# Performance work log

Hardware: AMD Instinct MI355X
Metric: run time of the kernel (lower is better)

Reference implementation:

```python
import jax, jax.numpy as jnp
import numpy as np

NDIGIT = 10
DIM_IN = 256
DIM_OUT = 784
BATCH = 16384


def setup_inputs() -> dict:
    key = jax.random.key(0)
    k_theta, k_label, k_W = jax.random.split(key, 3)
    theta = jax.random.normal(k_theta, (BATCH, DIM_IN), dtype=jnp.float32)
    label = jax.random.randint(k_label, (BATCH,), 0, NDIGIT, dtype=jnp.int32)
    # xavier_uniform for each (dim_out, dim_in) matrix
    limit = float(np.sqrt(6.0 / (DIM_IN + DIM_OUT)))
    megaW = jax.random.uniform(k_W, (NDIGIT, DIM_OUT, DIM_IN), dtype=jnp.float32,
                               minval=-limit, maxval=limit)
    megab = jnp.zeros((NDIGIT, DIM_OUT), dtype=jnp.float32)
    return {"theta": theta, "label": label, "megaW": megaW, "megab": megab}


def reference(theta, label, megaW, megab):
    # Dense compute across all 10 digit experts (matches torch.bmm over repeated theta)
    # added: [b, ndigit, dim_out]
    added = jnp.einsum('ndi,bi->bnd', megaW, theta) + megab[None, :, :]
    # Select the expert output per example by label (vector_gather)
    selected = jnp.take_along_axis(added, label[:, None, None].astype(jnp.int32), axis=1)[:, 0, :]
    probs = jax.nn.sigmoid(selected)
    return probs
```

## Files before the change

### kernel.cpp

```cpp
#include <hip/hip_runtime.h>
#include <hip/hip_bf16.h>

#define NDIGIT 10
#define DIM_IN 256
#define DIM_OUT 784
#define BATCH 16384
#define BM 64
#define BN 112
#define NCB 7
#define MAX_MT (BATCH / BM + NDIGIT)
#define GEMM_BLOCKS (MAX_MT * NCB)

#define WS_IDX 1024
#define WS_WBF_BYTES 69632

typedef __attribute__((ext_vector_type(4))) float f32x4;
typedef __attribute__((ext_vector_type(8))) short bf16x8;

__device__ __forceinline__ short f2bf(float f) {
    union { float f; unsigned u; } c; c.f = f;
    unsigned u = c.u;
    u += 0x7fffu + ((u >> 16) & 1u);
    return (short)(u >> 16);
}

__device__ __forceinline__ void gload16(const void* gp, void* lp) {
    __builtin_amdgcn_global_load_lds(
        (const __attribute__((address_space(1))) void*)gp,
        (__attribute__((address_space(3))) void*)lp, 16, 0, 0);
}

__global__ void prep_k(const float* __restrict__ megaW,
                       const int* __restrict__ label,
                       int* __restrict__ wsi,
                       short* __restrict__ wbf) {
    int b = blockIdx.x, t = threadIdx.x;
    if (b < 980) {
        int base = b * 2048 + t * 8;
        f32x4 v0 = *(const f32x4*)(megaW + base);
        f32x4 v1 = *(const f32x4*)(megaW + base + 4);
        bf16x8 o;
        o[0] = f2bf(v0[0]); o[1] = f2bf(v0[1]); o[2] = f2bf(v0[2]); o[3] = f2bf(v0[3]);
        o[4] = f2bf(v1[0]); o[5] = f2bf(v1[1]); o[6] = f2bf(v1[2]); o[7] = f2bf(v1[3]);
        *(bf16x8*)(wbf + base) = o;
    } else {
        __shared__ int h[NDIGIT];
        int j = b - 980;
        if (t < NDIGIT) h[t] = 0;
        __syncthreads();
        int i0 = j * 512;
        atomicAdd(&h[label[i0 + t]], 1);
        atomicAdd(&h[label[i0 + 256 + t]], 1);
        __syncthreads();
        if (t < NDIGIT) wsi[64 + j * 16 + t] = h[t];
    }
}

__global__ void scatter2_k(const int* __restrict__ label, int* __restrict__ wsi) {
    __shared__ int tot[NDIGIT], bef[NDIGIT], base[NDIGIT + 1], cur[NDIGIT];
    int j = blockIdx.x, t = threadIdx.x;
    if (t < NDIGIT) {
        int s = 0, sb = 0;
        for (int jj = 0; jj < 32; ++jj) {
            int v = wsi[64 + jj * 16 + t];
            s += v;
            if (jj < j) sb += v;
        }
        tot[t] = s; bef[t] = sb;
    }
    __syncthreads();
    if (t == 0) {
        int off = 0;
        for (int g = 0; g < NDIGIT; ++g) { base[g] = off; off += tot[g]; }
        base[NDIGIT] = off;
    }
    __syncthreads();
    if (t < NDIGIT) cur[t] = base[t] + bef[t];
    __syncthreads();
    int i = j * 512 + t;
    int g = label[i];
    int r = atomicAdd(&cur[g], 1);
    wsi[WS_IDX + r] = i;
    if (j == 0 && t == 0) {
        int off = 0, toff = 0;
        for (int g2 = 0; g2 < NDIGIT; ++g2) {
            wsi[g2] = off; wsi[12 + g2] = toff;
            off += tot[g2]; toff += (tot[g2] + BM - 1) / BM;
        }
        wsi[10] = off; wsi[22] = toff; wsi[24] = toff;
    }
}

__launch_bounds__(256, 4)
__global__ void moe_gemm4_k(const float* __restrict__ theta,
                            const float* __restrict__ megab,
                            const int* __restrict__ wsi,
                            const short* __restrict__ wbf,
                            float* __restrict__ out) {
    __shared__ short Bs[BN * 128];

    int Bid = blockIdx.x;
    const int q = GEMM_BLOCKS / 8, r = GEMM_BLOCKS % 8;
    int xcd = Bid & 7, slot = Bid >> 3;
    int w = (xcd < r ? xcd * (q + 1) : r * (q + 1) + (xcd - r) * q) + slot;
    int mt = w / NCB, cb = w % NCB;

    int total = wsi[24];
    if (mt >= total) return;

    int g = 0;
    while (mt >= wsi[12 + g + 1]) ++g;
    int lt    = mt - wsi[12 + g];
    int start = wsi[g];
    int cnt   = wsi[g + 1] - start;
    int row0  = lt * BM;
    int rc    = min(BM, cnt - row0);

    int tid = threadIdx.x;
    int wv = tid >> 6, l = tid & 63, r16 = l & 15, kg = l >> 4;

    const char* Wcb = (const char*)(wbf + ((size_t)g * DIM_OUT + (size_t)cb * BN) * DIM_IN);

#pragma unroll
    for (int it = 0; it < 7; ++it) {
        int lbyte = (it * 256 + tid) << 4;
        int L = lbyte ^ (((lbyte >> 8) & 7) << 4);
        int srcoff = ((L >> 8) << 9) + (L & 255);
        gload16(Wcb + srcoff, (char*)Bs + lbyte);
    }

    const int* idxlist = wsi + WS_IDX + start + row0;
    int mloc = wv * 16 + r16;
    int asrc = (mloc < rc) ? idxlist[mloc] : idxlist[0];
    const float* Arow = theta + (size_t)asrc * DIM_IN;
    bf16x8 a[8];
#pragma unroll
    for (int ks = 0; ks < 8; ++ks) {
        int k0 = ks * 32 + kg * 8;
        f32x4 v0 = *(const f32x4*)(Arow + k0);
        f32x4 v1 = *(const f32x4*)(Arow + k0 + 4);
        bf16x8 af;
        af[0] = f2bf(v0[0]); af[1] = f2bf(v0[1]);
        af[2] = f2bf(v0[2]); af[3] = f2bf(v0[3]);
        af[4] = f2bf(v1[0]); af[5] = f2bf(v1[1]);
        af[6] = f2bf(v1[2]); af[7] = f2bf(v1[3]);
        a[ks] = af;
    }

    f32x4 acc[NCB];
#pragma unroll
    for (int ns = 0; ns < NCB; ++ns) acc[ns] = (f32x4){0.f, 0.f, 0.f, 0.f};

    __syncthreads();
#pragma unroll
    for (int ks = 0; ks < 4; ++ks)
#pragma unroll
        for (int ns = 0; ns < NCB; ++ns) {
            int n = ns * 16 + r16;
            int byte = (n << 8) + (ks << 6) + (kg << 4);
            byte ^= (n & 7) << 4;
            bf16x8 b = *(const bf16x8*)((const char*)Bs + byte);
            acc[ns] = __builtin_amdgcn_mfma_f32_16x16x32_bf16(a[ks], b, acc[ns], 0, 0, 0);
        }
    __syncthreads();

#pragma unroll
    for (int it = 0; it < 7; ++it) {
        int lbyte = (it * 256 + tid) << 4;
        int L = lbyte ^ (((lbyte >> 8) & 7) << 4);
        int srcoff = ((L >> 8) << 9) + (L & 255) + 256;
        gload16(Wcb + srcoff, (char*)Bs + lbyte);
    }
    __syncthreads();

#pragma unroll
    for (int ks = 0; ks < 4; ++ks)
#pragma unroll
        for (int ns = 0; ns < NCB; ++ns) {
            int n = ns * 16 + r16;
            int byte = (n << 8) + (ks << 6) + (kg << 4);
            byte ^= (n & 7) << 4;
            bf16x8 b = *(const bf16x8*)((const char*)Bs + byte);
            acc[ns] = __builtin_amdgcn_mfma_f32_16x16x32_bf16(a[4 + ks], b, acc[ns], 0, 0, 0);
        }

    const float* bg = megab + (size_t)g * DIM_OUT + (size_t)cb * BN;
    int rbase = wv * 16 + kg * 4;
    int orow[4];
#pragma unroll
    for (int j = 0; j < 4; ++j)
        orow[j] = (rbase + j < rc) ? idxlist[rbase + j] : -1;

#pragma unroll
    for (int ns = 0; ns < NCB; ++ns) {
        int nloc = ns * 16 + r16;
        float bias = bg[nloc];
#pragma unroll
        for (int j = 0; j < 4; ++j) {
            if (orow[j] >= 0) {
                float x = acc[ns][j] + bias;
                out[(size_t)orow[j] * DIM_OUT + cb * BN + nloc] = 1.0f / (1.0f + __expf(-x));
            }
        }
    }
}

extern "C" void kernel_launch(void* const* d_in, const int* in_sizes, int n_in,
                              void* d_out, int out_size, void* d_ws, size_t ws_size,
                              hipStream_t stream) {
    const float* theta = (const float*)d_in[0];
    const int*   label = (const int*)d_in[1];
    const float* megaW = (const float*)d_in[2];
    const float* megab = (const float*)d_in[3];
    float* out = (float*)d_out;
    int* wsi = (int*)d_ws;
    short* wbf = (short*)((char*)d_ws + WS_WBF_BYTES);

    prep_k    <<<1012, 256, 0, stream>>>(megaW, label, wsi, wbf);
    scatter2_k<<<32, 512, 0, stream>>>(label, wsi);
    moe_gemm4_k<<<GEMM_BLOCKS, 256, 0, stream>>>(theta, megab, wsi, wbf, out);
}
```

Measured before the change: 47.83 us.

## Pre-gather theta to sorted bf16 and double-buffer W tiles in GEMM

Adds a kernel that gathers theta rows into label-sorted order and converts them to bf16 in workspace, so the GEMM reads contiguous bf16 A rows instead of converting fp32 in every N-column block. The GEMM splits K into four quarters staged through two LDS buffers, with explicit waitcnt and barriers so global-to-LDS loads overlap MFMA work. This costs an extra launch and an extra write and read of the sorted activations. The new path only runs when the workspace is large enough; otherwise it falls back to the old kernel.

```diff
diff --git a/kernel.cpp b/kernel.cpp
--- a/kernel.cpp
+++ b/kernel.cpp
@@ -10,9 +10,13 @@
 #define NCB 7
 #define MAX_MT (BATCH / BM + NDIGIT)
 #define GEMM_BLOCKS (MAX_MT * NCB)
+#define QBYTES 14336
 
 #define WS_IDX 1024
 #define WS_WBF_BYTES 69632
+#define WS_TH_BYTES (WS_WBF_BYTES + 2007040 * 2)
+#define WS_NEED_OLD (WS_TH_BYTES)
+#define WS_NEED_NEW (WS_TH_BYTES + BATCH * DIM_IN * 2)
 
 typedef __attribute__((ext_vector_type(4))) float f32x4;
 typedef __attribute__((ext_vector_type(8))) short bf16x8;
@@ -91,18 +95,61 @@
     }
 }
 
+__global__ void gth_k(const float* __restrict__ theta,
+                      const int* __restrict__ wsi,
+                      short* __restrict__ thsort) {
+    int gid = blockIdx.x * 256 + threadIdx.x;
+    int r = gid >> 5;
+    int c8 = (gid & 31) << 3;
+    int src = wsi[WS_IDX + r];
+    const float* p = theta + (size_t)src * DIM_IN + c8;
+    f32x4 v0 = *(const f32x4*)p;
+    f32x4 v1 = *(const f32x4*)(p + 4);
+    bf16x8 o;
+    o[0] = f2bf(v0[0]); o[1] = f2bf(v0[1]); o[2] = f2bf(v0[2]); o[3] = f2bf(v0[3]);
+    o[4] = f2bf(v1[0]); o[5] = f2bf(v1[1]); o[6] = f2bf(v1[2]); o[7] = f2bf(v1[3]);
+    *(bf16x8*)(thsort + (size_t)r * DIM_IN + c8) = o;
+}
+
+__device__ __forceinline__ void stage_q(const char* Wcb, int q, char* Bq, int tid) {
+#pragma unroll
+    for (int it = 0; it < 4; ++it) {
+        int chunk = it * 256 + tid;
+        if (chunk >= 896) chunk -= 128;
+        int lbyte = chunk << 4;
+        int L = lbyte ^ ((((lbyte >> 7) & 7)) << 4);
+        int row = L >> 7, koff = L & 127;
+        gload16(Wcb + row * 512 + q * 128 + koff, Bq + lbyte);
+    }
+}
+
+#define COMPUTE(Q, BUF) do { \
+    _Pragma("unroll") \
+    for (int ksl = 0; ksl < 2; ++ksl) { \
+        _Pragma("unroll") \
+        for (int ns = 0; ns < NCB; ++ns) { \
+            int n = ns * 16 + r16; \
+            int byte = (n << 7) + (ksl << 6) + (kg << 4); \
+            byte ^= (n & 7) << 4; \
+            bf16x8 bfr = *(const bf16x8*)((const char*)(BUF) + byte); \
+            acc[ns] = __builtin_amdgcn_mfma_f32_16x16x32_bf16(a[(Q) * 2 + ksl], bfr, acc[ns], 0, 0, 0); \
+        } \
+    } \
+} while (0)
+
 __launch_bounds__(256, 4)
-__global__ void moe_gemm4_k(const float* __restrict__ theta,
+__global__ void moe_gemm5_k(const short* __restrict__ thsort,
                             const float* __restrict__ megab,
                             const int* __restrict__ wsi,
                             const short* __restrict__ wbf,
                             float* __restrict__ out) {
-    __shared__ short Bs[BN * 128];
+    __shared__ char Bs0[QBYTES];
+    __shared__ char Bs1[QBYTES];
 
     int Bid = blockIdx.x;
-    const int q = GEMM_BLOCKS / 8, r = GEMM_BLOCKS % 8;
+    const int q8 = GEMM_BLOCKS / 8, r8 = GEMM_BLOCKS % 8;
     int xcd = Bid & 7, slot = Bid >> 3;
-    int w = (xcd < r ? xcd * (q + 1) : r * (q + 1) + (xcd - r) * q) + slot;
+    int w = (xcd < r8 ? xcd * (q8 + 1) : r8 * (q8 + 1) + (xcd - r8) * q8) + slot;
     int mt = w / NCB, cb = w % NCB;
 
     int total = wsi[24];
@@ -119,20 +166,108 @@
     int tid = threadIdx.x;
     int wv = tid >> 6, l = tid & 63, r16 = l & 15, kg = l >> 4;
 
+    int arow = start + row0 + wv * 16 + r16;
+    if (arow > BATCH - 1) arow = BATCH - 1;
+    const short* Ar = thsort + (size_t)arow * DIM_IN + kg * 8;
+    bf16x8 a[8];
+#pragma unroll
+    for (int ks = 0; ks < 8; ++ks)
+        a[ks] = *(const bf16x8*)(Ar + ks * 32);
+
+    const int* idxlist = wsi + WS_IDX + start + row0;
+    int rbase = wv * 16 + kg * 4;
+    int orow[4];
+#pragma unroll
+    for (int j = 0; j < 4; ++j)
+        orow[j] = (rbase + j < rc) ? idxlist[rbase + j] : -1;
+
     const char* Wcb = (const char*)(wbf + ((size_t)g * DIM_OUT + (size_t)cb * BN) * DIM_IN);
 
+    stage_q(Wcb, 0, Bs0, tid);
+    stage_q(Wcb, 1, Bs1, tid);
+
+    f32x4 acc[NCB];
+#pragma unroll
+    for (int ns = 0; ns < NCB; ++ns) acc[ns] = (f32x4){0.f, 0.f, 0.f, 0.f};
+
+    asm volatile("s_waitcnt vmcnt(4)" ::: "memory");
+    __builtin_amdgcn_s_barrier();
+    __builtin_amdgcn_sched_barrier(0);
+
+    COMPUTE(0, Bs0);
+    asm volatile("s_waitcnt lgkmcnt(0)" ::: "memory");
+    __builtin_amdgcn_s_barrier();
+    stage_q(Wcb, 2, Bs0, tid);
+    asm volatile("s_waitcnt vmcnt(4)" ::: "memory");
+    __builtin_amdgcn_s_barrier();
+    __builtin_amdgcn_sched_barrier(0);
+
+    COMPUTE(1, Bs1);
+    asm volatile("s_waitcnt lgkmcnt(0)" ::: "memory");
+    __builtin_amdgcn_s_barrier();
+    stage_q(Wcb, 3, Bs1, tid);
+    asm volatile("s_waitcnt vmcnt(4)" ::: "memory");
+    __builtin_amdgcn_s_barrier();
+    __builtin_amdgcn_sched_barrier(0);
+
+    COMPUTE(2, Bs0);
+    asm volatile("s_waitcnt lgkmcnt(0) vmcnt(0)" ::: "memory");
+    __builtin_amdgcn_s_barrier();
+    __builtin_amdgcn_sched_barrier(0);
+
+    COMPUTE(3, Bs1);
+
+    const float* bg = megab + (size_t)g * DIM_OUT + (size_t)cb * BN;
+#pragma unroll
+    for (int ns = 0; ns < NCB; ++ns) {
+        int nloc = ns * 16 + r16;
+        float bias = bg[nloc];
+#pragma unroll
+        for (int j = 0; j < 4; ++j) {
+            if (orow[j] >= 0) {
+                float x = acc[ns][j] + bias;
+                out[(size_t)orow[j] * DIM_OUT + cb * BN + nloc] = 1.0f / (1.0f + __expf(-x));
+            }
+        }
+    }
+}
+
+__launch_bounds__(256, 4)
+__global__ void moe_gemm4_k(const float* __restrict__ theta,
+                            const float* __restrict__ megab,
+                            const int* __restrict__ wsi,
+                            const short* __restrict__ wbf,
+                            float* __restrict__ out) {
+    __shared__ short Bsf[BN * 128];
+    int Bid = blockIdx.x;
+    const int q8 = GEMM_BLOCKS / 8, r8 = GEMM_BLOCKS % 8;
+    int xcd = Bid & 7, slot = Bid >> 3;
+    int w = (xcd < r8 ? xcd * (q8 + 1) : r8 * (q8 + 1) + (xcd - r8) * q8) + slot;
+    int mt = w / NCB, cb = w % NCB;
+    int total = wsi[24];
+    if (mt >= total) return;
+    int g = 0;
+    while (mt >= wsi[12 + g + 1]) ++g;
+    int lt    = mt - wsi[12 + g];
+    int start = wsi[g];
+    int cnt   = wsi[g + 1] - start;
+    int row0  = lt * BM;
+    int rc    = min(BM, cnt - row0);
+    int tid = threadIdx.x;
+    int wv = tid >> 6, l = tid & 63, r16 = l & 15, kg = l >> 4;
+    const char* Wcb = (const char*)(wbf + ((size_t)g * DIM_OUT + (size_t)cb * BN) * DIM_IN);
 #pragma unroll
     for (int it = 0; it < 7; ++it) {
         int lbyte = (it * 256 + tid) << 4;
         int L = lbyte ^ (((lbyte >> 8) & 7) << 4);
         int srcoff = ((L >> 8) << 9) + (L & 255);
-        gload16(Wcb + srcoff, (char*)Bs + lbyte);
-    }
-
+        gload16(Wcb + srcoff, (char*)Bsf + lbyte);
+    }
     const int* idxlist = wsi + WS_IDX + start + row0;
     int mloc = wv * 16 + r16;
     int asrc = (mloc < rc) ? idxlist[mloc] : idxlist[0];
-    const float* Arow = theta + (size_t)asrc * DIM_IN;
+    const float* Arow = (const float*)0;
+    Arow = theta + (size_t)asrc * DIM_IN;
     bf16x8 a[8];
 #pragma unroll
     for (int ks = 0; ks < 8; ++ks) {
@@ -146,11 +281,9 @@
         af[6] = f2bf(v1[2]); af[7] = f2bf(v1[3]);
         a[ks] = af;
     }
-
     f32x4 acc[NCB];
 #pragma unroll
     for (int ns = 0; ns < NCB; ++ns) acc[ns] = (f32x4){0.f, 0.f, 0.f, 0.f};
-
     __syncthreads();
 #pragma unroll
     for (int ks = 0; ks < 4; ++ks)
@@ -159,20 +292,18 @@
             int n = ns * 16 + r16;
             int byte = (n << 8) + (ks << 6) + (kg << 4);
             byte ^= (n & 7) << 4;
-            bf16x8 b = *(const bf16x8*)((const char*)Bs + byte);
+            bf16x8 b = *(const bf16x8*)((const char*)Bsf + byte);
             acc[ns] = __builtin_amdgcn_mfma_f32_16x16x32_bf16(a[ks], b, acc[ns], 0, 0, 0);
         }
     __syncthreads();
-
 #pragma unroll
     for (int it = 0; it < 7; ++it) {
         int lbyte = (it * 256 + tid) << 4;
         int L = lbyte ^ (((lbyte >> 8) & 7) << 4);
         int srcoff = ((L >> 8) << 9) + (L & 255) + 256;
-        gload16(Wcb + srcoff, (char*)Bs + lbyte);
-    }
-    __syncthreads();
-
+        gload16(Wcb + srcoff, (char*)Bsf + lbyte);
+    }
+    __syncthreads();
 #pragma unroll
     for (int ks = 0; ks < 4; ++ks)
 #pragma unroll
@@ -180,17 +311,15 @@
             int n = ns * 16 + r16;
             int byte = (n << 8) + (ks << 6) + (kg << 4);
             byte ^= (n & 7) << 4;
-            bf16x8 b = *(const bf16x8*)((const char*)Bs + byte);
+            bf16x8 b = *(const bf16x8*)((const char*)Bsf + byte);
             acc[ns] = __builtin_amdgcn_mfma_f32_16x16x32_bf16(a[4 + ks], b, acc[ns], 0, 0, 0);
         }
-
     const float* bg = megab + (size_t)g * DIM_OUT + (size_t)cb * BN;
     int rbase = wv * 16 + kg * 4;
     int orow[4];
 #pragma unroll
     for (int j = 0; j < 4; ++j)
         orow[j] = (rbase + j < rc) ? idxlist[rbase + j] : -1;
-
 #pragma unroll
     for (int ns = 0; ns < NCB; ++ns) {
         int nloc = ns * 16 + r16;
@@ -218,5 +347,12 @@
 
     prep_k    <<<1012, 256, 0, stream>>>(megaW, label, wsi, wbf);
     scatter2_k<<<32, 512, 0, stream>>>(label, wsi);
-    moe_gemm4_k<<<GEMM_BLOCKS, 256, 0, stream>>>(theta, megab, wsi, wbf, out);
-}
+
+    if (ws_size >= (size_t)WS_NEED_NEW) {
+        short* thsort = (short*)((char*)d_ws + WS_TH_BYTES);
+        gth_k     <<<2048, 256, 0, stream>>>(theta, wsi, thsort);
+        moe_gemm5_k<<<GEMM_BLOCKS, 256, 0, stream>>>(thsort, megab, wsi, wbf, out);
+    } else {
+        moe_gemm4_k<<<GEMM_BLOCKS, 256, 0, stream>>>(theta, megab, wsi, wbf, out);
+    }
+}
```

After: 47.19 us. Within noise of the previous version (-1.3%).

## Pre-gather theta to sorted bf16 and reuse full-K weight tile across 256 rows

Applied to the files above, without the earlier changes.

Adds a gather kernel that writes theta rows in label-sorted order as bf16, then a new GEMM kernel where each block keeps both K-halves of a 112-column weight slice in double LDS buffers. That slice is reused across four 64-row subtiles (256 rows), with register double-buffering of A loads and epilogue overlap. This cuts repeated weight staging and per-block fp32 theta conversion, but costs an extra kernel launch, an extra pass over theta, and lower occupancy. It falls back to the old kernel when the workspace is too small.

```diff
diff --git a/kernel.cpp b/kernel.cpp
--- a/kernel.cpp
+++ b/kernel.cpp
@@ -10,9 +10,14 @@
 #define NCB 7
 #define MAX_MT (BATCH / BM + NDIGIT)
 #define GEMM_BLOCKS (MAX_MT * NCB)
+#define MAX_CHUNKS (BATCH / 256 + NDIGIT)
+#define G6_BLOCKS (MAX_CHUNKS * NCB)
+#define HBYTES 28672
 
 #define WS_IDX 1024
 #define WS_WBF_BYTES 69632
+#define WS_TH_BYTES (WS_WBF_BYTES + 2007040 * 2)
+#define WS_NEED_NEW (WS_TH_BYTES + BATCH * DIM_IN * 2)
 
 typedef __attribute__((ext_vector_type(4))) float f32x4;
 typedef __attribute__((ext_vector_type(8))) short bf16x8;
@@ -82,13 +87,178 @@
     int r = atomicAdd(&cur[g], 1);
     wsi[WS_IDX + r] = i;
     if (j == 0 && t == 0) {
-        int off = 0, toff = 0;
+        int off = 0, toff = 0, choff = 0;
         for (int g2 = 0; g2 < NDIGIT; ++g2) {
-            wsi[g2] = off; wsi[12 + g2] = toff;
-            off += tot[g2]; toff += (tot[g2] + BM - 1) / BM;
+            wsi[g2] = off; wsi[12 + g2] = toff; wsi[26 + g2] = choff;
+            off += tot[g2];
+            toff += (tot[g2] + BM - 1) / BM;
+            choff += (tot[g2] + 255) / 256;
         }
         wsi[10] = off; wsi[22] = toff; wsi[24] = toff;
-    }
+        wsi[36] = choff; wsi[38] = choff;
+    }
+}
+
+__global__ void gth_k(const float* __restrict__ theta,
+                      const int* __restrict__ wsi,
+                      short* __restrict__ thsort) {
+    int gid = blockIdx.x * 256 + threadIdx.x;
+    int r = gid >> 5;
+    int c8 = (gid & 31) << 3;
+    int src = wsi[WS_IDX + r];
+    const float* p = theta + (size_t)src * DIM_IN + c8;
+    f32x4 v0 = *(const f32x4*)p;
+    f32x4 v1 = *(const f32x4*)(p + 4);
+    bf16x8 o;
+    o[0] = f2bf(v0[0]); o[1] = f2bf(v0[1]); o[2] = f2bf(v0[2]); o[3] = f2bf(v0[3]);
+    o[4] = f2bf(v1[0]); o[5] = f2bf(v1[1]); o[6] = f2bf(v1[2]); o[7] = f2bf(v1[3]);
+    *(bf16x8*)(thsort + (size_t)r * DIM_IN + c8) = o;
+}
+
+
+#define LOADA(A, T) do {                                                       \
+    int arow_ = start + row0 + (T) * 64 + wv * 16 + r16;                       \
+    int amax_ = start + cnt - 1;                                               \
+    if (arow_ > amax_) arow_ = amax_;                                          \
+    const short* Ar_ = thsort + (size_t)arow_ * DIM_IN + kg * 8;               \
+    _Pragma("unroll")                                                          \
+    for (int ks = 0; ks < 8; ++ks) (A)[ks] = *(const bf16x8*)(Ar_ + ks * 32);  \
+} while (0)
+
+#define LOADO(O, T) do {                                                       \
+    const int* idxl_ = wsi + WS_IDX + start + row0 + (T) * 64;                 \
+    _Pragma("unroll")                                                          \
+    for (int j = 0; j < 4; ++j) {                                              \
+        int rl_ = (T) * 64 + rb + j;                                           \
+        (O)[j] = (rl_ < cnt - row0) ? idxl_[rb + j] : -1;                      \
+    }                                                                          \
+} while (0)
+
+#define CMPH(H, A, BUF) do {                                                   \
+    _Pragma("unroll")                                                          \
+    for (int ksl = 0; ksl < 4; ++ksl) {                                        \
+        _Pragma("unroll")                                                      \
+        for (int ns = 0; ns < NCB; ++ns) {                                     \
+            int n_ = ns * 16 + r16;                                            \
+            int byte_ = (n_ << 8) + (ksl << 6) + (kg << 4);                    \
+            byte_ ^= (n_ & 7) << 4;                                            \
+            bf16x8 bfr_ = *(const bf16x8*)((const char*)(BUF) + byte_);        \
+            acc[ns] = __builtin_amdgcn_mfma_f32_16x16x32_bf16(                 \
+                (A)[(H) * 4 + ksl], bfr_, acc[ns], 0, 0, 0);                   \
+        }                                                                      \
+    }                                                                          \
+} while (0)
+
+#define ZACC() do {                                                            \
+    _Pragma("unroll")                                                          \
+    for (int ns = 0; ns < NCB; ++ns) acc[ns] = (f32x4){0.f, 0.f, 0.f, 0.f};   \
+} while (0)
+
+#define EPI(O) do {                                                            \
+    _Pragma("unroll")                                                          \
+    for (int ns = 0; ns < NCB; ++ns) {                                         \
+        int nloc_ = ns * 16 + r16;                                             \
+        _Pragma("unroll")                                                      \
+        for (int j = 0; j < 4; ++j) {                                          \
+            if ((O)[j] >= 0) {                                                 \
+                float x_ = acc[ns][j] + biasv[ns];                             \
+                out[(size_t)(O)[j] * DIM_OUT + cb * BN + nloc_] =              \
+                    1.0f / (1.0f + __expf(-x_));                               \
+            }                                                                  \
+        }                                                                      \
+    }                                                                          \
+} while (0)
+
+#define STAGEH(H, BUF) do {                                                    \
+    _Pragma("unroll")                                                          \
+    for (int it = 0; it < 7; ++it) {                                           \
+        int lbyte_ = (it * 256 + tid) << 4;                                    \
+        int L_ = lbyte_ ^ (((lbyte_ >> 8) & 7) << 4);                          \
+        int src_ = ((L_ >> 8) << 9) + (L_ & 255) + (H) * 256;                  \
+        gload16(Wcb + src_, (char*)(BUF) + lbyte_);                            \
+    }                                                                          \
+} while (0)
+
+__launch_bounds__(256, 2)
+__global__ void moe_gemm6_k(const short* __restrict__ thsort,
+                            const float* __restrict__ megab,
+                            const int* __restrict__ wsi,
+                            const short* __restrict__ wbf,
+                            float* __restrict__ out) {
+    __shared__ char Bs0[HBYTES];
+    __shared__ char Bs1[HBYTES];
+
+    int Bid = blockIdx.x;
+    const int q8 = G6_BLOCKS / 8, r8 = G6_BLOCKS % 8;
+    int xcd = Bid & 7, slot = Bid >> 3;
+    int w = (xcd < r8 ? xcd * (q8 + 1) : r8 * (q8 + 1) + (xcd - r8) * q8) + slot;
+    int ct = w / NCB, cb = w % NCB;
+
+    int ctotal = wsi[38];
+    if (ct >= ctotal) return;
+
+    int tid = threadIdx.x;
+    int wv = tid >> 6, l = tid & 63, r16 = l & 15, kg = l >> 4;
+    int rb = wv * 16 + kg * 4;
+
+    int coff = (l < 11) ? wsi[26 + l] : 0x7fffffff;
+    int boff = (l < 11) ? wsi[l] : 0;
+    unsigned long long m = __ballot(ct >= coff);
+    int g = __popcll(m) - 1;
+    int lc    = ct - __shfl(coff, g);
+    int start = __shfl(boff, g);
+    int cnt   = __shfl(boff, g + 1) - start;
+    int row0  = lc * 256;
+
+    const char* Wcb = (const char*)(wbf + ((size_t)g * DIM_OUT + (size_t)cb * BN) * DIM_IN);
+
+    bf16x8 a0[8], a1[8];
+    int or0[4], or1[4];
+    LOADA(a0, 0);
+    LOADO(or0, 0);
+    float biasv[NCB];
+    {
+        const float* bg = megab + (size_t)g * DIM_OUT + cb * BN;
+#pragma unroll
+        for (int ns = 0; ns < NCB; ++ns) biasv[ns] = bg[ns * 16 + r16];
+    }
+
+    STAGEH(0, Bs0);
+    STAGEH(1, Bs1);
+
+    f32x4 acc[NCB];
+    ZACC();
+
+    asm volatile("s_waitcnt vmcnt(7)" ::: "memory");
+    __builtin_amdgcn_s_barrier();
+    __builtin_amdgcn_sched_barrier(0);
+
+    CMPH(0, a0, Bs0);
+
+    asm volatile("s_waitcnt vmcnt(0)" ::: "memory");
+    __builtin_amdgcn_s_barrier();
+    __builtin_amdgcn_sched_barrier(0);
+
+    LOADA(a1, 1); LOADO(or1, 1);
+    CMPH(1, a0, Bs1);
+    EPI(or0);
+
+    ZACC();
+    LOADA(a0, 2); LOADO(or0, 2);
+    CMPH(0, a1, Bs0);
+    CMPH(1, a1, Bs1);
+    EPI(or1);
+
+    ZACC();
+    LOADA(a1, 3); LOADO(or1, 3);
+    CMPH(0, a0, Bs0);
+    CMPH(1, a0, Bs1);
+    EPI(or0);
+
+    ZACC();
+    CMPH(0, a1, Bs0);
+    CMPH(1, a1, Bs1);
+    EPI(or1);
 }
 
 __launch_bounds__(256, 4)
@@ -97,17 +267,14 @@
                             const int* __restrict__ wsi,
                             const short* __restrict__ wbf,
                             float* __restrict__ out) {
-    __shared__ short Bs[BN * 128];
-
+    __shared__ short Bsf[BN * 128];
     int Bid = blockIdx.x;
-    const int q = GEMM_BLOCKS / 8, r = GEMM_BLOCKS % 8;
+    const int q8 = GEMM_BLOCKS / 8, r8 = GEMM_BLOCKS % 8;
     int xcd = Bid & 7, slot = Bid >> 3;
-    int w = (xcd < r ? xcd * (q + 1) : r * (q + 1) + (xcd - r) * q) + slot;
+    int w = (xcd < r8 ? xcd * (q8 + 1) : r8 * (q8 + 1) + (xcd - r8) * q8) + slot;
     int mt = w / NCB, cb = w % NCB;
-
     int total = wsi[24];
     if (mt >= total) return;
-
     int g = 0;
     while (mt >= wsi[12 + g + 1]) ++g;
     int lt    = mt - wsi[12 + g];
@@ -115,20 +282,16 @@
     int cnt   = wsi[g + 1] - start;
     int row0  = lt * BM;
     int rc    = min(BM, cnt - row0);
-
     int tid = threadIdx.x;
     int wv = tid >> 6, l = tid & 63, r16 = l & 15, kg = l >> 4;
-
     const char* Wcb = (const char*)(wbf + ((size_t)g * DIM_OUT + (size_t)cb * BN) * DIM_IN);
-
 #pragma unroll
     for (int it = 0; it < 7; ++it) {
         int lbyte = (it * 256 + tid) << 4;
         int L = lbyte ^ (((lbyte >> 8) & 7) << 4);
         int srcoff = ((L >> 8) << 9) + (L & 255);
-        gload16(Wcb + srcoff, (char*)Bs + lbyte);
-    }
-
+        gload16(Wcb + srcoff, (char*)Bsf + lbyte);
+    }
     const int* idxlist = wsi + WS_IDX + start + row0;
     int mloc = wv * 16 + r16;
     int asrc = (mloc < rc) ? idxlist[mloc] : idxlist[0];
@@ -146,11 +309,9 @@
         af[6] = f2bf(v1[2]); af[7] = f2bf(v1[3]);
         a[ks] = af;
     }
-
     f32x4 acc[NCB];
 #pragma unroll
     for (int ns = 0; ns < NCB; ++ns) acc[ns] = (f32x4){0.f, 0.f, 0.f, 0.f};
-
     __syncthreads();
 #pragma unroll
     for (int ks = 0; ks < 4; ++ks)
@@ -159,20 +320,18 @@
             int n = ns * 16 + r16;
             int byte = (n << 8) + (ks << 6) + (kg << 4);
             byte ^= (n & 7) << 4;
-            bf16x8 b = *(const bf16x8*)((const char*)Bs + byte);
+            bf16x8 b = *(const bf16x8*)((const char*)Bsf + byte);
             acc[ns] = __builtin_amdgcn_mfma_f32_16x16x32_bf16(a[ks], b, acc[ns], 0, 0, 0);
         }
     __syncthreads();
-
 #pragma unroll
     for (int it = 0; it < 7; ++it) {
         int lbyte = (it * 256 + tid) << 4;
         int L = lbyte ^ (((lbyte >> 8) & 7) << 4);
         int srcoff = ((L >> 8) << 9) + (L & 255) + 256;
-        gload16(Wcb + srcoff, (char*)Bs + lbyte);
-    }
-    __syncthreads();
-
+        gload16(Wcb + srcoff, (char*)Bsf + lbyte);
+    }
+    __syncthreads();
 #pragma unroll
     for (int ks = 0; ks < 4; ++ks)
 #pragma unroll
@@ -180,17 +339,15 @@
             int n = ns * 16 + r16;
             int byte = (n << 8) + (ks << 6) + (kg << 4);
             byte ^= (n & 7) << 4;
-            bf16x8 b = *(const bf16x8*)((const char*)Bs + byte);
+            bf16x8 b = *(const bf16x8*)((const char*)Bsf + byte);
             acc[ns] = __builtin_amdgcn_mfma_f32_16x16x32_bf16(a[4 + ks], b, acc[ns], 0, 0, 0);
         }
-
     const float* bg = megab + (size_t)g * DIM_OUT + (size_t)cb * BN;
     int rbase = wv * 16 + kg * 4;
     int orow[4];
 #pragma unroll
     for (int j = 0; j < 4; ++j)
         orow[j] = (rbase + j < rc) ? idxlist[rbase + j] : -1;
-
 #pragma unroll
     for (int ns = 0; ns < NCB; ++ns) {
         int nloc = ns * 16 + r16;
@@ -218,5 +375,12 @@
 
     prep_k    <<<1012, 256, 0, stream>>>(megaW, label, wsi, wbf);
     scatter2_k<<<32, 512, 0, stream>>>(label, wsi);
-    moe_gemm4_k<<<GEMM_BLOCKS, 256, 0, stream>>>(theta, megab, wsi, wbf, out);
-}
+
+    if (ws_size >= (size_t)WS_NEED_NEW) {
+        short* thsort = (short*)((char*)d_ws + WS_TH_BYTES);
+        gth_k     <<<2048, 256, 0, stream>>>(theta, wsi, thsort);
+        moe_gemm6_k<<<G6_BLOCKS, 256, 0, stream>>>(thsort, megab, wsi, wbf, out);
+    } else {
+        moe_gemm4_k<<<GEMM_BLOCKS, 256, 0, stream>>>(theta, megab, wsi, wbf, out);
+    }
+}
```

Result: slower. 74.36 us (+55.5%).

## Pre-gather sorted bf16 theta, precompute tile descriptors, stage W in quarters

Applied to the files above, without the earlier changes.

Adds a gather kernel that writes theta rows in label-sorted order as bf16, so the GEMM reads contiguous half-size A rows instead of converting fp32 per tile, which each of the 7 column blocks repeated. scatter2 now writes a packed per-tile descriptor, so the GEMM no longer loops to find its expert. The W tile is staged in four 14KB K-quarters to cut LDS use, and launch bounds are raised to 8 blocks per CU for occupancy. The cost is an extra kernel launch, a round trip through workspace memory, and more barriers per tile.

```diff
diff --git a/kernel.cpp b/kernel.cpp
--- a/kernel.cpp
+++ b/kernel.cpp
@@ -9,10 +9,13 @@
 #define BN 112
 #define NCB 7
 #define MAX_MT (BATCH / BM + NDIGIT)
-#define GEMM_BLOCKS (MAX_MT * NCB)
+#define G9_BLOCKS (MAX_MT * NCB)
+#define QB 14336
 
 #define WS_IDX 1024
+#define WS_DESC 600
 #define WS_WBF_BYTES 69632
+#define WS_TH_BYTES (WS_WBF_BYTES + 2007040 * 2)
 
 typedef __attribute__((ext_vector_type(4))) float f32x4;
 typedef __attribute__((ext_vector_type(8))) short bf16x8;
@@ -57,7 +60,7 @@
 }
 
 __global__ void scatter2_k(const int* __restrict__ label, int* __restrict__ wsi) {
-    __shared__ int tot[NDIGIT], bef[NDIGIT], base[NDIGIT + 1], cur[NDIGIT];
+    __shared__ int tot[NDIGIT], bef[NDIGIT], base[NDIGIT + 1], cur[NDIGIT], toff[NDIGIT + 1];
     int j = blockIdx.x, t = threadIdx.x;
     if (t < NDIGIT) {
         int s = 0, sb = 0;
@@ -70,126 +73,131 @@
     }
     __syncthreads();
     if (t == 0) {
-        int off = 0;
-        for (int g = 0; g < NDIGIT; ++g) { base[g] = off; off += tot[g]; }
-        base[NDIGIT] = off;
+        int off = 0, tf = 0;
+        for (int g = 0; g < NDIGIT; ++g) {
+            base[g] = off; toff[g] = tf;
+            off += tot[g]; tf += (tot[g] + BM - 1) / BM;
+        }
+        base[NDIGIT] = off; toff[NDIGIT] = tf;
     }
     __syncthreads();
     if (t < NDIGIT) cur[t] = base[t] + bef[t];
+    if (j == 0) {
+        int ptotal = toff[NDIGIT];
+        for (int p = t; p < ptotal; p += 512) {
+            int g2 = 0;
+            while (p >= toff[g2 + 1]) ++g2;
+            int row0 = (p - toff[g2]) * BM;
+            int rcv = tot[g2] - row0; if (rcv > BM) rcv = BM;
+            wsi[WS_DESC + p] = (base[g2] + row0) | (rcv << 14) | (g2 << 21);
+        }
+        if (t == 0) wsi[24] = ptotal;
+    }
     __syncthreads();
     int i = j * 512 + t;
     int g = label[i];
     int r = atomicAdd(&cur[g], 1);
     wsi[WS_IDX + r] = i;
-    if (j == 0 && t == 0) {
-        int off = 0, toff = 0;
-        for (int g2 = 0; g2 < NDIGIT; ++g2) {
-            wsi[g2] = off; wsi[12 + g2] = toff;
-            off += tot[g2]; toff += (tot[g2] + BM - 1) / BM;
-        }
-        wsi[10] = off; wsi[22] = toff; wsi[24] = toff;
-    }
-}
-
-__launch_bounds__(256, 4)
-__global__ void moe_gemm4_k(const float* __restrict__ theta,
+    if (j == 0 && t < NDIGIT) wsi[t] = base[t];
+    if (j == 0 && t == 0) wsi[10] = base[NDIGIT];
+}
+
+__global__ void gth_k(const float* __restrict__ theta,
+                      const int* __restrict__ wsi,
+                      short* __restrict__ thsort) {
+    int gid = blockIdx.x * 256 + threadIdx.x;
+    int r = gid >> 5;
+    int c8 = (gid & 31) << 3;
+    int src = wsi[WS_IDX + r];
+    const float* p = theta + (size_t)src * DIM_IN + c8;
+    f32x4 v0 = *(const f32x4*)p;
+    f32x4 v1 = *(const f32x4*)(p + 4);
+    bf16x8 o;
+    o[0] = f2bf(v0[0]); o[1] = f2bf(v0[1]); o[2] = f2bf(v0[2]); o[3] = f2bf(v0[3]);
+    o[4] = f2bf(v1[0]); o[5] = f2bf(v1[1]); o[6] = f2bf(v1[2]); o[7] = f2bf(v1[3]);
+    *(bf16x8*)(thsort + (size_t)r * DIM_IN + c8) = o;
+}
+
+__device__ __forceinline__ void stage_q(const char* Wcb, int q, char* Bq, int tid) {
+#pragma unroll
+    for (int it = 0; it < 4; ++it) {
+        int chunk = it * 256 + tid;
+        if (chunk >= 896) chunk -= 128;
+        int lbyte = chunk << 4;
+        int L = lbyte ^ ((((lbyte >> 7) & 7)) << 4);
+        int row = L >> 7, koff = L & 127;
+        gload16(Wcb + row * 512 + q * 128 + koff, Bq + lbyte);
+    }
+}
+
+#define COMPUTE(Q) do {                                                        \
+    _Pragma("unroll")                                                          \
+    for (int ksl = 0; ksl < 2; ++ksl) {                                        \
+        _Pragma("unroll")                                                      \
+        for (int ns = 0; ns < NCB; ++ns) {                                     \
+            int n_ = ns * 16 + r16;                                            \
+            int byte_ = (n_ << 7) + (ksl << 6) + (kg << 4);                    \
+            byte_ ^= (n_ & 7) << 4;                                            \
+            bf16x8 bfr_ = *(const bf16x8*)(Bs + byte_);                        \
+            acc[ns] = __builtin_amdgcn_mfma_f32_16x16x32_bf16(                 \
+                a[(Q) * 2 + ksl], bfr_, acc[ns], 0, 0, 0);                     \
+        }                                                                      \
+    }                                                                          \
+} while (0)
+
+__launch_bounds__(256, 8)
+__global__ void moe_gemm9_k(const short* __restrict__ thsort,
                             const float* __restrict__ megab,
                             const int* __restrict__ wsi,
                             const short* __restrict__ wbf,
                             float* __restrict__ out) {
-    __shared__ short Bs[BN * 128];
+    __shared__ char Bs[QB];
 
     int Bid = blockIdx.x;
-    const int q = GEMM_BLOCKS / 8, r = GEMM_BLOCKS % 8;
+    const int q8 = G9_BLOCKS / 8, r8 = G9_BLOCKS % 8;
     int xcd = Bid & 7, slot = Bid >> 3;
-    int w = (xcd < r ? xcd * (q + 1) : r * (q + 1) + (xcd - r) * q) + slot;
+    int w = (xcd < r8 ? xcd * (q8 + 1) : r8 * (q8 + 1) + (xcd - r8) * q8) + slot;
     int mt = w / NCB, cb = w % NCB;
 
     int total = wsi[24];
     if (mt >= total) return;
 
-    int g = 0;
-    while (mt >= wsi[12 + g + 1]) ++g;
-    int lt    = mt - wsi[12 + g];
-    int start = wsi[g];
-    int cnt   = wsi[g + 1] - start;
-    int row0  = lt * BM;
-    int rc    = min(BM, cnt - row0);
+    int d = wsi[WS_DESC + mt];
+    int startRow = d & 0x3FFF;
+    int rc = (d >> 14) & 0x7F;
+    int g  = d >> 21;
 
     int tid = threadIdx.x;
     int wv = tid >> 6, l = tid & 63, r16 = l & 15, kg = l >> 4;
 
+    int mloc = wv * 16 + r16; if (mloc >= rc) mloc = rc - 1;
+    const short* Ar = thsort + (size_t)(startRow + mloc) * DIM_IN + kg * 8;
+    bf16x8 a[8];
+#pragma unroll
+    for (int ks = 0; ks < 8; ++ks)
+        a[ks] = *(const bf16x8*)(Ar + ks * 32);
+
     const char* Wcb = (const char*)(wbf + ((size_t)g * DIM_OUT + (size_t)cb * BN) * DIM_IN);
 
-#pragma unroll
-    for (int it = 0; it < 7; ++it) {
-        int lbyte = (it * 256 + tid) << 4;
-        int L = lbyte ^ (((lbyte >> 8) & 7) << 4);
-        int srcoff = ((L >> 8) << 9) + (L & 255);
-        gload16(Wcb + srcoff, (char*)Bs + lbyte);
-    }
-
-    const int* idxlist = wsi + WS_IDX + start + row0;
-    int mloc = wv * 16 + r16;
-    int asrc = (mloc < rc) ? idxlist[mloc] : idxlist[0];
-    const float* Arow = theta + (size_t)asrc * DIM_IN;
-    bf16x8 a[8];
-#pragma unroll
-    for (int ks = 0; ks < 8; ++ks) {
-        int k0 = ks * 32 + kg * 8;
-        f32x4 v0 = *(const f32x4*)(Arow + k0);
-        f32x4 v1 = *(const f32x4*)(Arow + k0 + 4);
-        bf16x8 af;
-        af[0] = f2bf(v0[0]); af[1] = f2bf(v0[1]);
-        af[2] = f2bf(v0[2]); af[3] = f2bf(v0[3]);
-        af[4] = f2bf(v1[0]); af[5] = f2bf(v1[1]);
-        af[6] = f2bf(v1[2]); af[7] = f2bf(v1[3]);
-        a[ks] = af;
-    }
-
     f32x4 acc[NCB];
 #pragma unroll
     for (int ns = 0; ns < NCB; ++ns) acc[ns] = (f32x4){0.f, 0.f, 0.f, 0.f};
 
-    __syncthreads();
-#pragma unroll
-    for (int ks = 0; ks < 4; ++ks)
-#pragma unroll
-        for (int ns = 0; ns < NCB; ++ns) {
-            int n = ns * 16 + r16;
-            int byte = (n << 8) + (ks << 6) + (kg << 4);
-            byte ^= (n & 7) << 4;
-            bf16x8 b = *(const bf16x8*)((const char*)Bs + byte);
-            acc[ns] = __builtin_amdgcn_mfma_f32_16x16x32_bf16(a[ks], b, acc[ns], 0, 0, 0);
-        }
-    __syncthreads();
-
-#pragma unroll
-    for (int it = 0; it < 7; ++it) {
-        int lbyte = (it * 256 + tid) << 4;
-        int L = lbyte ^ (((lbyte >> 8) & 7) << 4);
-        int srcoff = ((L >> 8) << 9) + (L & 255) + 256;
-        gload16(Wcb + srcoff, (char*)Bs + lbyte);
-    }
-    __syncthreads();
-
-#pragma unroll
-    for (int ks = 0; ks < 4; ++ks)
-#pragma unroll
-        for (int ns = 0; ns < NCB; ++ns) {
-            int n = ns * 16 + r16;
-            int byte = (n << 8) + (ks << 6) + (kg << 4);
-            byte ^= (n & 7) << 4;
-            bf16x8 b = *(const bf16x8*)((const char*)Bs + byte);
-            acc[ns] = __builtin_amdgcn_mfma_f32_16x16x32_bf16(a[4 + ks], b, acc[ns], 0, 0, 0);
-        }
+#pragma unroll
+    for (int q = 0; q < 4; ++q) {
+        stage_q(Wcb, q, Bs, tid);
+        __syncthreads();
+        COMPUTE(q);
+        if (q < 3) __syncthreads();
+    }
 
     const float* bg = megab + (size_t)g * DIM_OUT + (size_t)cb * BN;
+    const int* idxl = wsi + WS_IDX + startRow;
     int rbase = wv * 16 + kg * 4;
     int orow[4];
 #pragma unroll
     for (int j = 0; j < 4; ++j)
-        orow[j] = (rbase + j < rc) ? idxlist[rbase + j] : -1;
+        orow[j] = (rbase + j < rc) ? idxl[rbase + j] : -1;
 
 #pragma unroll
     for (int ns = 0; ns < NCB; ++ns) {
@@ -214,9 +222,11 @@
     const float* megab = (const float*)d_in[3];
     float* out = (float*)d_out;
     int* wsi = (int*)d_ws;
-    short* wbf = (short*)((char*)d_ws + WS_WBF_BYTES);
+    short* wbf    = (short*)((char*)d_ws + WS_WBF_BYTES);
+    short* thsort = (short*)((char*)d_ws + WS_TH_BYTES);
 
     prep_k    <<<1012, 256, 0, stream>>>(megaW, label, wsi, wbf);
     scatter2_k<<<32, 512, 0, stream>>>(label, wsi);
-    moe_gemm4_k<<<GEMM_BLOCKS, 256, 0, stream>>>(theta, megab, wsi, wbf, out);
-}
+    gth_k     <<<2048, 256, 0, stream>>>(theta, wsi, thsort);
+    moe_gemm9_k<<<G9_BLOCKS, 256, 0, stream>>>(thsort, megab, wsi, wbf, out);
+}
```

Result: slower. 52.63 us (+10.1%).
